# Kernel optimization log

Hardware: AMD Instinct MI355X
Metric: run time of the kernel (lower is better)

Reference implementation:

```python
import jax, jax.numpy as jnp
import numpy as np

ALPHA = 0.2  # LeakyReLU negative slope
N, F_IN, F_OUT = 8192, 512, 64
NEG_BIG = -9e15


def setup_inputs() -> dict:
    key = jax.random.key(0)
    k1, k2, k3, k4 = jax.random.split(key, 4)
    h = jax.random.normal(k1, (N, F_IN), dtype=jnp.float32)
    # xavier_uniform with gain 1.414
    lim_w = 1.414 * np.sqrt(6.0 / (F_IN + F_OUT))
    W = jax.random.uniform(k2, (F_IN, F_OUT), dtype=jnp.float32, minval=-lim_w, maxval=lim_w)
    lim_a = 1.414 * np.sqrt(6.0 / (2 * F_OUT + 1))
    a = jax.random.uniform(k3, (2 * F_OUT, 1), dtype=jnp.float32, minval=-lim_a, maxval=lim_a)
    adj = jax.random.randint(k4, (N, N), 0, 2, dtype=jnp.int32)
    return {"h": h, "W": W, "a": a, "adj": adj}


def reference(h, W, a, adj):
    Wh = h @ W                                  # [N, F_OUT]
    f_out = Wh.shape[1]
    a1 = a[:f_out, 0]                            # source half of attention vector
    a2 = a[f_out:, 0]                            # target half
    # e_ij = LeakyReLU(Wh_i . a1 + Wh_j . a2); equals cat([Wh_i, Wh_j]) @ a
    e = jax.nn.leaky_relu(jnp.matmul(Wh, a1)[:, None] + jnp.matmul(Wh, a2)[None, :], ALPHA)  # [N, N]
    attention = jnp.where(adj > 0, e, NEG_BIG)
    attention = jax.nn.softmax(attention, axis=1)
    # dropout is a no-op at inference (training=False)
    h_prime = attention @ Wh                     # [N, F_OUT]
    return jax.nn.elu(h_prime)                   # concat=True -> ELU
```

## Files before the change

### kernel.cpp

```cpp
#include <hip/hip_runtime.h>
#include <hip/hip_bf16.h>


typedef _Float16 f16;
typedef _Float16 f16x2 __attribute__((ext_vector_type(2)));
typedef _Float16 f16x4 __attribute__((ext_vector_type(4)));
typedef _Float16 f16x8 __attribute__((ext_vector_type(8)));
typedef float f32x4 __attribute__((ext_vector_type(4)));
typedef int   i32x4 __attribute__((ext_vector_type(4)));

#define GAT_N 8192
#define GAT_FIN 512
#define GAT_FOUT 64
#define GAT_ALPHA 0.2f

__global__ void k0_wtrans(const float* __restrict__ W, f16* __restrict__ WT) {
    int idx = blockIdx.x * blockDim.x + threadIdx.x;
    int k = idx >> 6, c = idx & 63;
    WT[c * GAT_FIN + k] = (f16)W[idx];
}

__global__ __launch_bounds__(256) void k1_gemm(const float* __restrict__ h,
        const f16* __restrict__ WT, const float* __restrict__ a,
        f16* __restrict__ WhT, float* __restrict__ s1, float* __restrict__ s2) {
    __shared__ float pacc[4][4][64][4];
    __shared__ float s1red[4][16], s2red[4][16];

    int tid = threadIdx.x;
    int w = tid >> 6, lane = tid & 63;
    int l15 = lane & 15, quad = lane >> 4;
    int rb = blockIdx.x * 16;
    size_t arow = (size_t)(rb + l15) * GAT_FIN;

    f32x4 acc[4] = {};
#pragma unroll
    for (int ks = 0; ks < 4; ks++) {
        int kb = w * 128 + ks * 32 + quad * 8;
        const float4* hp = (const float4*)(h + arow + kb);
        float4 h0 = hp[0], h1 = hp[1];
        f16x8 af = { (f16)h0.x, (f16)h0.y, (f16)h0.z, (f16)h0.w,
                     (f16)h1.x, (f16)h1.y, (f16)h1.z, (f16)h1.w };
#pragma unroll
        for (int t = 0; t < 4; t++) {
            f16x8 bf = *(const f16x8*)(WT + (t * 16 + l15) * GAT_FIN + kb);
            acc[t] = __builtin_amdgcn_mfma_f32_16x16x32_f16(af, bf, acc[t], 0, 0, 0);
        }
    }
#pragma unroll
    for (int t = 0; t < 4; t++)
        *(f32x4*)&pacc[w][t][lane][0] = acc[t];
    __syncthreads();

    float a1v = a[w * 16 + l15];
    float a2v = a[GAT_FOUT + w * 16 + l15];
    float vreg[4];
#pragma unroll
    for (int reg = 0; reg < 4; reg++) {
        float v = 0.f;
#pragma unroll
        for (int ww = 0; ww < 4; ww++) v += pacc[ww][w][lane][reg];
        vreg[reg] = v;
    }
    f16x4 pk = { (f16)vreg[0], (f16)vreg[1], (f16)vreg[2], (f16)vreg[3] };
    *(f16x4*)(WhT + (size_t)(w * 16 + l15) * GAT_N + rb + quad * 4) = pk;

#pragma unroll
    for (int reg = 0; reg < 4; reg++) {
        float c1 = vreg[reg] * a1v, c2 = vreg[reg] * a2v;
#pragma unroll
        for (int off = 1; off < 16; off <<= 1) {
            c1 += __shfl_xor(c1, off);
            c2 += __shfl_xor(c2, off);
        }
        if (l15 == 0) { s1red[w][quad * 4 + reg] = c1; s2red[w][quad * 4 + reg] = c2; }
    }
    __syncthreads();
    if (tid < 16) {
        float t1 = 0.f, t2 = 0.f;
#pragma unroll
        for (int ww = 0; ww < 4; ww++) { t1 += s1red[ww][tid]; t2 += s2red[ww][tid]; }
        s1[rb + tid] = t1;
        s2[rb + tid] = t2;
    }
}

__global__ __launch_bounds__(512, 4) void k3_attn(const int* __restrict__ adj,
        const f16* __restrict__ WhT, const float* __restrict__ s1,
        const float* __restrict__ s2, float* __restrict__ out) {
    __shared__ __align__(16) char smem[2 * 16 * 520 * 2];
    f16* pbuf = (f16*)smem;
    float (*accbuf)[16][64] = (float (*)[16][64])smem;
    __shared__ float dbuf2[16];
    __shared__ float mred[8];

    int tid = threadIdx.x;
    int w = tid >> 6, lane = tid & 63;
    int l15 = lane & 15, quad = lane >> 4;
    int hhalf = lane >> 5, q = lane & 31;
    int rb = blockIdx.x * 16;
    int r = 2 * w + hhalf;

    float m = -1e30f;
    for (int i = tid; i < GAT_N; i += 512) m = fmaxf(m, s2[i]);
#pragma unroll
    for (int off = 32; off >= 1; off >>= 1) m = fmaxf(m, __shfl_xor(m, off));
    if (lane == 0) mred[w] = m;
    __syncthreads();
    float mxv = mred[0];
#pragma unroll
    for (int ww = 1; ww < 8; ww++) mxv = fmaxf(mxv, mred[ww]);

    float s1r = s1[rb + r];
    float cr = s1r + mxv;
    cr = fmaxf(cr, GAT_ALPHA * cr);
    const int* adjrow = adj + (size_t)(rb + r) * GAT_N;

    float dacc = 0.f;
    f32x4 acc[4] = {};
    i32x4  av[4];
    float4 sv[4];

    auto stage = [&](int bb) {
#pragma unroll
        for (int p = 0; p < 4; p++) {
            float svv[4] = { sv[p].x, sv[p].y, sv[p].z, sv[p].w };
            int base = (4 * p + (q >> 3)) * 520 + ((q >> 1) & 3) * 128 + r * 8 + (q & 1) * 4;
            f16 pf[4];
#pragma unroll
            for (int j = 0; j < 4; j++) {
                float e = s1r + svv[j];
                e = fmaxf(e, GAT_ALPHA * e);
                float pv = __expf(e - cr);
                pv = (av[p][j] > 0) ? pv : 0.0f;
                dacc += pv;
                pf[j] = (f16)pv;
            }
            f16x2 lo = { pf[0], pf[1] }, hi = { pf[2], pf[3] };
            *(f16x2*)&pbuf[bb * 8320 + base]     = lo;
            *(f16x2*)&pbuf[bb * 8320 + base + 2] = hi;
        }
    };

#pragma unroll
    for (int p = 0; p < 4; p++) {
        int c0 = p * 128 + q * 4;
        av[p] = __builtin_nontemporal_load((const i32x4*)(adjrow + c0));
        sv[p] = *(const float4*)(s2 + c0);
    }
    stage(0);
    __syncthreads();

    for (int rd = 0; rd < 16; rd++) {
        int b = rd & 1;
        if (rd < 15) {
#pragma unroll
            for (int p = 0; p < 4; p++) {
                int c0 = (rd + 1) * 512 + p * 128 + q * 4;
                av[p] = __builtin_nontemporal_load((const i32x4*)(adjrow + c0));
                sv[p] = *(const float4*)(s2 + c0);
            }
        }
#pragma unroll
        for (int sl = 0; sl < 2; sl++) {
            int s_loc = 2 * w + sl;
            f16x8 af = *(const f16x8*)&pbuf[b * 8320 + s_loc * 520 + lane * 8];
            int kb = rd * 512 + s_loc * 32 + quad * 8;
#pragma unroll
            for (int t = 0; t < 4; t++) {
                f16x8 bf = *(const f16x8*)(WhT + (size_t)(t * 16 + l15) * GAT_N + kb);
                acc[t] = __builtin_amdgcn_mfma_f32_16x16x32_f16(af, bf, acc[t], 0, 0, 0);
            }
        }
        if (rd < 15) stage(1 - b);
        __syncthreads();
    }

#pragma unroll
    for (int t = 0; t < 4; t++)
#pragma unroll
        for (int reg = 0; reg < 4; reg++)
            accbuf[w][quad * 4 + reg][t * 16 + l15] = acc[t][reg];
#pragma unroll
    for (int off = 16; off >= 1; off >>= 1) dacc += __shfl_xor(dacc, off);
    if (q == 0) dbuf2[r] = dacc;
    __syncthreads();

    for (int o = tid; o < 16 * 64; o += 512) {
        int rr = o >> 6, c = o & 63;
        float num = 0.f;
#pragma unroll
        for (int ww = 0; ww < 8; ww++) num += accbuf[ww][rr][c];
        float hp = num / dbuf2[rr];
        out[(size_t)(rb + rr) * GAT_FOUT + c] = hp > 0.f ? hp : expm1f(hp);
    }
}

extern "C" void kernel_launch(void* const* d_in, const int* in_sizes, int n_in,
                              void* d_out, int out_size, void* d_ws, size_t ws_size,
                              hipStream_t stream) {
    const float* h   = (const float*)d_in[0];
    const float* W   = (const float*)d_in[1];
    const float* a   = (const float*)d_in[2];
    const int*   adj = (const int*)d_in[3];
    float* out = (float*)d_out;

    char* ws = (char*)d_ws;
    f16*   WT  = (f16*)ws;
    f16*   WhT = (f16*)(ws + 65536);
    float* s1  = (float*)(ws + 65536 + 1048576);
    float* s2  = (float*)(ws + 65536 + 1048576 + 32768);

    k0_wtrans<<<128, 256, 0, stream>>>(W, WT);
    k1_gemm<<<512, 256, 0, stream>>>(h, WT, a, WhT, s1, s2);
    k3_attn<<<512, 512, 0, stream>>>(adj, WhT, s1, s2, out);
}
```

Measured before the change: 410.3 us.

## Prefetch adjacency two rounds ahead with double register sets in attention kernel

Adjacency and s2 loads are now issued two rounds ahead, using two alternating register sets and a loop unrolled by two. WhT fragments are loaded into registers before the MFMAs, and the exponential is rewritten as exp2 with a fused multiply-add. The aim is to hide global-memory latency on the adjacency stream. The extra registers come at the cost of relaxing launch bounds to 2 blocks per SM, which may reduce occupancy.

```diff
diff --git a/kernel.cpp b/kernel.cpp
--- a/kernel.cpp
+++ b/kernel.cpp
@@ -13,6 +13,7 @@
 #define GAT_FIN 512
 #define GAT_FOUT 64
 #define GAT_ALPHA 0.2f
+#define GAT_L2E 1.44269504088896340736f
 
 __global__ void k0_wtrans(const float* __restrict__ W, f16* __restrict__ WT) {
     int idx = blockIdx.x * blockDim.x + threadIdx.x;
@@ -84,7 +85,7 @@
     }
 }
 
-__global__ __launch_bounds__(512, 4) void k3_attn(const int* __restrict__ adj,
+__global__ __launch_bounds__(512, 2) void k3_attn(const int* __restrict__ adj,
         const f16* __restrict__ WhT, const float* __restrict__ s1,
         const float* __restrict__ s2, float* __restrict__ out) {
     __shared__ __align__(16) char smem[2 * 16 * 520 * 2];
@@ -113,66 +114,74 @@
     float s1r = s1[rb + r];
     float cr = s1r + mxv;
     cr = fmaxf(cr, GAT_ALPHA * cr);
+    float mcrl = -cr * GAT_L2E;
     const int* adjrow = adj + (size_t)(rb + r) * GAT_N;
 
     float dacc = 0.f;
     f32x4 acc[4] = {};
-    i32x4  av[4];
-    float4 sv[4];
-
-    auto stage = [&](int bb) {
+    i32x4  avA[4], avB[4];
+    float4 svA[4], svB[4];
+
+    auto loadreg = [&](i32x4 (&av_)[4], float4 (&sv_)[4], int rd) {
 #pragma unroll
         for (int p = 0; p < 4; p++) {
-            float svv[4] = { sv[p].x, sv[p].y, sv[p].z, sv[p].w };
+            int c0 = rd * 512 + p * 128 + q * 4;
+            av_[p] = __builtin_nontemporal_load((const i32x4*)(adjrow + c0));
+            sv_[p] = *(const float4*)(s2 + c0);
+        }
+    };
+
+    auto stage = [&](const i32x4 (&av_)[4], const float4 (&sv_)[4], int bb) {
+#pragma unroll
+        for (int p = 0; p < 4; p++) {
+            float svv[4] = { sv_[p].x, sv_[p].y, sv_[p].z, sv_[p].w };
             int base = (4 * p + (q >> 3)) * 520 + ((q >> 1) & 3) * 128 + r * 8 + (q & 1) * 4;
             f16 pf[4];
 #pragma unroll
             for (int j = 0; j < 4; j++) {
-                float e = s1r + svv[j];
-                e = fmaxf(e, GAT_ALPHA * e);
-                float pv = __expf(e - cr);
-                pv = (av[p][j] > 0) ? pv : 0.0f;
+                float x = s1r + svv[j];
+                float e = fmaxf(x, GAT_ALPHA * x);
+                float pv = exp2f(fmaf(e, GAT_L2E, mcrl));
+                pv = (av_[p][j] > 0) ? pv : 0.0f;
                 dacc += pv;
                 pf[j] = (f16)pv;
             }
-            f16x2 lo = { pf[0], pf[1] }, hi = { pf[2], pf[3] };
-            *(f16x2*)&pbuf[bb * 8320 + base]     = lo;
-            *(f16x2*)&pbuf[bb * 8320 + base + 2] = hi;
+            f16x4 pk = { pf[0], pf[1], pf[2], pf[3] };
+            *(f16x4*)&pbuf[bb * 8320 + base] = pk;
         }
     };
 
-#pragma unroll
-    for (int p = 0; p < 4; p++) {
-        int c0 = p * 128 + q * 4;
-        av[p] = __builtin_nontemporal_load((const i32x4*)(adjrow + c0));
-        sv[p] = *(const float4*)(s2 + c0);
-    }
-    stage(0);
-    __syncthreads();
-
-    for (int rd = 0; rd < 16; rd++) {
-        int b = rd & 1;
-        if (rd < 15) {
-#pragma unroll
-            for (int p = 0; p < 4; p++) {
-                int c0 = (rd + 1) * 512 + p * 128 + q * 4;
-                av[p] = __builtin_nontemporal_load((const i32x4*)(adjrow + c0));
-                sv[p] = *(const float4*)(s2 + c0);
-            }
-        }
+    auto round = [&](int rd, int b, const i32x4 (&avP)[4], const float4 (&svP)[4],
+                     i32x4 (&avF)[4], float4 (&svF)[4]) {
+        f16x8 bfr[2][4];
 #pragma unroll
         for (int sl = 0; sl < 2; sl++) {
-            int s_loc = 2 * w + sl;
-            f16x8 af = *(const f16x8*)&pbuf[b * 8320 + s_loc * 520 + lane * 8];
-            int kb = rd * 512 + s_loc * 32 + quad * 8;
-#pragma unroll
-            for (int t = 0; t < 4; t++) {
-                f16x8 bf = *(const f16x8*)(WhT + (size_t)(t * 16 + l15) * GAT_N + kb);
-                acc[t] = __builtin_amdgcn_mfma_f32_16x16x32_f16(af, bf, acc[t], 0, 0, 0);
-            }
-        }
-        if (rd < 15) stage(1 - b);
+            int kb = rd * 512 + (2 * w + sl) * 32 + quad * 8;
+#pragma unroll
+            for (int t = 0; t < 4; t++)
+                bfr[sl][t] = *(const f16x8*)(WhT + (size_t)(t * 16 + l15) * GAT_N + kb);
+        }
+        if (rd < 14) loadreg(avF, svF, rd + 2);
+#pragma unroll
+        for (int sl = 0; sl < 2; sl++) {
+            f16x8 af = *(const f16x8*)&pbuf[b * 8320 + (2 * w + sl) * 520 + lane * 8];
+#pragma unroll
+            for (int t = 0; t < 4; t++)
+                acc[t] = __builtin_amdgcn_mfma_f32_16x16x32_f16(af, bfr[sl][t], acc[t], 0, 0, 0);
+        }
+        if (rd < 15) stage(avP, svP, 1 - b);
         __syncthreads();
+    };
+
+    loadreg(avA, svA, 0);
+    stage(avA, svA, 0);
+    loadreg(avB, svB, 1);
+    __syncthreads();
+
+#pragma unroll 1
+    for (int rd = 0; rd < 16; rd += 2) {
+        round(rd,     0, avB, svB, avA, svA);
+        round(rd + 1, 1, avA, svA, avB, svB);
     }
 
 #pragma unroll
```

After: 427.1 us. 1.04x slower.
